# Performance work log

Measured on AMD Instinct MI355X. Metric: run time of the kernel, lower is better.

Reference implementation:

```python
import jax, jax.numpy as jnp
import numpy as np

N = 100000
E = 1200000


def _gcn_norm(edge_index, num_nodes):
    # Add self-loops and compute symmetric normalization (PyG GCNConv default).
    row = jnp.concatenate([edge_index[0], jnp.arange(num_nodes, dtype=edge_index.dtype)])
    col = jnp.concatenate([edge_index[1], jnp.arange(num_nodes, dtype=edge_index.dtype)])
    deg = jax.ops.segment_sum(jnp.ones_like(col, dtype=jnp.float32), col, num_segments=num_nodes)
    dinv = jnp.where(deg > 0, jax.lax.rsqrt(jnp.maximum(deg, 1.0)), 0.0)
    norm = dinv[row] * dinv[col]  # [E+N]
    return row, col, norm


def _gcn_conv(x, W, b, row, col, norm, num_nodes):
    h = x @ W                      # [N, out] dense transform first (fewer bytes to gather)
    msg = h[row] * norm[:, None]   # gather + edge-wise scale
    out = jax.ops.segment_sum(msg, col, num_segments=num_nodes)  # scatter-add to targets
    return out + b


def setup_inputs() -> dict:
    key = jax.random.key(0)
    k1, k2, k3, k4 = jax.random.split(key, 4)
    x = jax.random.normal(k1, (N, 128), dtype=jnp.float32)
    edge_index = jax.random.randint(k2, (2, E), 0, N, dtype=jnp.int64)
    W1 = jax.random.normal(k3, (128, 256), dtype=jnp.float32) * (1.0 / np.sqrt(128))
    b1 = jnp.zeros((256,), dtype=jnp.float32)
    W2 = jax.random.normal(k4, (256, 40), dtype=jnp.float32) * (1.0 / np.sqrt(256))
    b2 = jnp.zeros((40,), dtype=jnp.float32)
    return {"x": x, "edge_index": edge_index, "W1": W1, "b1": b1, "W2": W2, "b2": b2}


def reference(x, edge_index, W1, b1, W2, b2):
    row, col, norm = _gcn_norm(edge_index, N)
    h = _gcn_conv(x, W1, b1, row, col, norm, N)
    h = jax.nn.relu(h)
    # dropout omitted: eval mode (training=False) is identity
    return _gcn_conv(h, W2, b2, row, col, norm, N)
```

## Files before the change

### kernel.cpp

```cpp
#include <hip/hip_runtime.h>
#include <hip/hip_bf16.h>

#define NN 100000
#define EE 1200000
#define F1 128
#define F2 256
#define F3 40
#define MROWS 64
#define NBUK ((NN + 255) / 256)
#define NBLK 256
#define CHUNK ((EE + NBLK - 1) / NBLK)
#define DCAP 4096
#define XB2 ((NN * 32 + 255) / 256)

typedef __bf16 bf16x8 __attribute__((ext_vector_type(8)));
typedef float  f32x4  __attribute__((ext_vector_type(4)));

__device__ __forceinline__ unsigned short f2bf(float f) {
    unsigned u = __float_as_uint(f);
    return (unsigned short)((u + 0x7fffu + ((u >> 16) & 1u)) >> 16);
}
__device__ __forceinline__ float bflo(unsigned v) { return __uint_as_float(v << 16); }
__device__ __forceinline__ float bfhi(unsigned v) { return __uint_as_float(v & 0xffff0000u); }

__global__ __launch_bounds__(256) void k_hist(const int* __restrict__ col,
                                              int* __restrict__ hist) {
    __shared__ int lh[NBUK];
    for (int i = threadIdx.x; i < NBUK; i += 256) lh[i] = 0;
    __syncthreads();
    int e0 = blockIdx.x * CHUNK;
    int e1 = min(e0 + CHUNK, EE);
    for (int e = e0 + threadIdx.x; e < e1; e += 256) {
        int c = col[e];
        if ((unsigned)c < (unsigned)NN) atomicAdd(&lh[c >> 8], 1);
    }
    __syncthreads();
    for (int i = threadIdx.x; i < NBUK; i += 256) hist[i * NBLK + blockIdx.x] = lh[i];
}

__global__ __launch_bounds__(256) void k_scanbin(int* __restrict__ hist,
                                                 int* __restrict__ bintot) {
    __shared__ int s[NBLK];
    int b = blockIdx.x;
    int v = hist[b * NBLK + threadIdx.x];
    s[threadIdx.x] = v;
    __syncthreads();
    int acc = v;
    for (int d = 1; d < NBLK; d <<= 1) {
        int add = (threadIdx.x >= d) ? s[threadIdx.x - d] : 0;
        __syncthreads();
        acc += add;
        s[threadIdx.x] = acc;
        __syncthreads();
    }
    hist[b * NBLK + threadIdx.x] = acc - v;
    if (threadIdx.x == NBLK - 1) bintot[b] = acc;
}

__global__ __launch_bounds__(512) void k_scanbase(const int* __restrict__ bintot,
                                                  int* __restrict__ binbase) {
    __shared__ int s[512];
    int v = (threadIdx.x < NBUK) ? bintot[threadIdx.x] : 0;
    s[threadIdx.x] = v;
    __syncthreads();
    int acc = v;
    for (int d = 1; d < 512; d <<= 1) {
        int add = (threadIdx.x >= d) ? s[threadIdx.x - d] : 0;
        __syncthreads();
        acc += add;
        s[threadIdx.x] = acc;
        __syncthreads();
    }
    if (threadIdx.x < NBUK) binbase[threadIdx.x] = acc - v;
    if (threadIdx.x == NBUK - 1) binbase[NBUK] = acc;
}

__global__ __launch_bounds__(256) void k_scat(const int* __restrict__ row,
                                              const int* __restrict__ col,
                                              const int* __restrict__ hist,
                                              const int* __restrict__ binbase,
                                              unsigned* __restrict__ rec) {
    __shared__ int lcur[NBUK];
    for (int i = threadIdx.x; i < NBUK; i += 256)
        lcur[i] = binbase[i] + hist[i * NBLK + blockIdx.x];
    __syncthreads();
    int e0 = blockIdx.x * CHUNK;
    int e1 = min(e0 + CHUNK, EE);
    for (int e = e0 + threadIdx.x; e < e1; e += 256) {
        int r = row[e], c = col[e];
        if ((unsigned)c < (unsigned)NN) {
            int pos = atomicAdd(&lcur[c >> 8], 1);
            rec[pos] = ((unsigned)r & 0xFFFFFFu) | ((unsigned)(c & 255) << 24);
        }
    }
}

__global__ __launch_bounds__(256) void k_csr(const int* __restrict__ binbase,
                                             const unsigned* __restrict__ rec,
                                             int* __restrict__ eidx,
                                             int* __restrict__ cnt,
                                             int* __restrict__ cursor,
                                             float* __restrict__ dinv) {
    __shared__ int lcnt[256];
    __shared__ int s[256];
    __shared__ int lcur[256];
    __shared__ int lde[DCAP];
    const int b = blockIdx.x;
    const int tid = threadIdx.x;
    lcnt[tid] = 0;
    __syncthreads();
    const int base = binbase[b];
    const int nb = min(binbase[b + 1] - base, DCAP);
    for (int j = tid; j < nb; j += 256) atomicAdd(&lcnt[rec[base + j] >> 24], 1);
    __syncthreads();
    int cv = lcnt[tid];
    s[tid] = cv;
    __syncthreads();
    int acc = cv;
    for (int d = 1; d < 256; d <<= 1) {
        int add = (tid >= d) ? s[tid - d] : 0;
        __syncthreads();
        acc += add;
        s[tid] = acc;
        __syncthreads();
    }
    int excl = acc - cv;
    lcur[tid] = excl;
    const int node = (b << 8) + tid;
    if (node < NN) {
        cnt[node] = cv;
        cursor[node] = base + excl + cv;
        dinv[node] = rsqrtf((float)(cv + 1));
    }
    __syncthreads();
    for (int j = tid; j < nb; j += 256) {
        unsigned v = rec[base + j];
        int pos = atomicAdd(&lcur[v >> 24], 1);
        lde[pos] = (int)(v & 0xFFFFFFu);
    }
    __syncthreads();
    for (int j = tid; j < nb; j += 256) eidx[base + j] = lde[j];
}

__global__ void k_prep(const float4* __restrict__ x, const float* __restrict__ dinv,
                       uint2* __restrict__ xh,
                       const float* __restrict__ W1, const float* __restrict__ W2,
                       __hip_bfloat16* __restrict__ W1p, __hip_bfloat16* __restrict__ W2p) {
    if (blockIdx.x < XB2) {
        int idx = blockIdx.x * 256 + threadIdx.x;
        float d = dinv[idx >> 5];
        float4 v = x[idx];
        uint2 o;
        o.x = (unsigned)f2bf(v.x * d) | ((unsigned)f2bf(v.y * d) << 16);
        o.y = (unsigned)f2bf(v.z * d) | ((unsigned)f2bf(v.w * d) << 16);
        xh[idx] = o;
    } else {
        int idx = (blockIdx.x - XB2) * 256 + threadIdx.x;
        if (idx < F1 * F2) {
            int k = idx / F2, col = idx - (idx / F2) * F2;
            int k8 = k >> 3, j = k & 7;
            W1p[((size_t)(k8 * F2 + col) << 3) + j] = __float2bfloat16(W1[(size_t)k * F2 + col]);
        } else if (idx < F1 * F2 + F2 * 48) {
            int i2 = idx - F1 * F2;
            int k = i2 / 48, col = i2 - (i2 / 48) * 48;
            int k8 = k >> 3, j = k & 7;
            float v = (col < F3) ? W2[(size_t)k * F3 + col] : 0.0f;
            W2p[((size_t)(k8 * 48 + col) << 3) + j] = __float2bfloat16(v);
        }
    }
}

__global__ __launch_bounds__(256) void k_agg1(const int* __restrict__ cursor,
                                              const int* __restrict__ cnt,
                                              const int* __restrict__ eidx,
                                              const float* __restrict__ dinv,
                                              const unsigned* __restrict__ xh,
                                              unsigned* __restrict__ agg) {
    int node = blockIdx.x * 4 + (threadIdx.x >> 6);
    int lane = threadIdx.x & 63;
    if (node >= NN) return;
    unsigned vs = xh[((size_t)node << 6) + lane];
    float a0 = bflo(vs), a1 = bfhi(vs);
    int n = cnt[node];
    int s = cursor[node] - n;
    int k = 0;
    for (; k + 7 < n; k += 8) {
        int r0 = eidx[s + k + 0], r1 = eidx[s + k + 1];
        int r2 = eidx[s + k + 2], r3 = eidx[s + k + 3];
        int r4 = eidx[s + k + 4], r5 = eidx[s + k + 5];
        int r6 = eidx[s + k + 6], r7 = eidx[s + k + 7];
        unsigned v0 = xh[((size_t)r0 << 6) + lane];
        unsigned v1 = xh[((size_t)r1 << 6) + lane];
        unsigned v2 = xh[((size_t)r2 << 6) + lane];
        unsigned v3 = xh[((size_t)r3 << 6) + lane];
        unsigned v4 = xh[((size_t)r4 << 6) + lane];
        unsigned v5 = xh[((size_t)r5 << 6) + lane];
        unsigned v6 = xh[((size_t)r6 << 6) + lane];
        unsigned v7 = xh[((size_t)r7 << 6) + lane];
        a0 += bflo(v0); a1 += bfhi(v0);
        a0 += bflo(v1); a1 += bfhi(v1);
        a0 += bflo(v2); a1 += bfhi(v2);
        a0 += bflo(v3); a1 += bfhi(v3);
        a0 += bflo(v4); a1 += bfhi(v4);
        a0 += bflo(v5); a1 += bfhi(v5);
        a0 += bflo(v6); a1 += bfhi(v6);
        a0 += bflo(v7); a1 += bfhi(v7);
    }
    for (; k + 3 < n; k += 4) {
        int r0 = eidx[s + k + 0], r1 = eidx[s + k + 1];
        int r2 = eidx[s + k + 2], r3 = eidx[s + k + 3];
        unsigned v0 = xh[((size_t)r0 << 6) + lane];
        unsigned v1 = xh[((size_t)r1 << 6) + lane];
        unsigned v2 = xh[((size_t)r2 << 6) + lane];
        unsigned v3 = xh[((size_t)r3 << 6) + lane];
        a0 += bflo(v0); a1 += bfhi(v0);
        a0 += bflo(v1); a1 += bfhi(v1);
        a0 += bflo(v2); a1 += bfhi(v2);
        a0 += bflo(v3); a1 += bfhi(v3);
    }
    for (; k < n; ++k) {
        unsigned v0 = xh[((size_t)eidx[s + k] << 6) + lane];
        a0 += bflo(v0); a1 += bfhi(v0);
    }
    float d = dinv[node];
    agg[((size_t)node << 6) + lane] = (unsigned)f2bf(a0 * d) | ((unsigned)f2bf(a1 * d) << 16);
}

__global__ __launch_bounds__(256) void k_gemm_mfma(
    const __hip_bfloat16* __restrict__ agg, const __hip_bfloat16* __restrict__ W1p,
    const float* __restrict__ b1, const __hip_bfloat16* __restrict__ W2p,
    const float* __restrict__ dinv, unsigned short* __restrict__ tg) {
    __shared__ __hip_bfloat16 h_s[MROWS][F2 + 8];
    const int i0   = blockIdx.x * MROWS;
    const int wave = threadIdx.x >> 6;
    const int lane = threadIdx.x & 63;
    const int m = lane & 15, q = lane >> 4;
    const int rowA = i0 + wave * 16 + m;

    f32x4 acc[16];
#pragma unroll
    for (int c = 0; c < 16; ++c) acc[c] = (f32x4){0.f, 0.f, 0.f, 0.f};

#pragma unroll
    for (int s = 0; s < 4; ++s) {
        bf16x8 a;
#pragma unroll
        for (int j = 0; j < 8; ++j) a[j] = (__bf16)0.0f;
        if (rowA < NN) a = *(const bf16x8*)(agg + (size_t)rowA * F1 + s * 32 + q * 8);
        const __hip_bfloat16* bp = W1p + ((size_t)(4 * s + q) * F2) * 8;
#pragma unroll
        for (int c = 0; c < 16; ++c) {
            bf16x8 b = *(const bf16x8*)(bp + ((size_t)(c * 16 + m) << 3));
            acc[c] = __builtin_amdgcn_mfma_f32_16x16x32_bf16(a, b, acc[c], 0, 0, 0);
        }
    }

#pragma unroll
    for (int c = 0; c < 16; ++c) {
        int col = c * 16 + m;
        float bj = b1[col];
#pragma unroll
        for (int r = 0; r < 4; ++r) {
            int lr = wave * 16 + q * 4 + r;
            h_s[lr][col] = __float2bfloat16(fmaxf(acc[c][r] + bj, 0.0f));
        }
    }
    __syncthreads();

    f32x4 acc2[3];
#pragma unroll
    for (int c = 0; c < 3; ++c) acc2[c] = (f32x4){0.f, 0.f, 0.f, 0.f};

#pragma unroll
    for (int s = 0; s < 8; ++s) {
        bf16x8 a = *(const bf16x8*)(&h_s[wave * 16 + m][s * 32 + q * 8]);
        const __hip_bfloat16* bp = W2p + ((size_t)(4 * s + q) * 48) * 8;
#pragma unroll
        for (int c = 0; c < 3; ++c) {
            bf16x8 b = *(const bf16x8*)(bp + ((size_t)(c * 16 + m) << 3));
            acc2[c] = __builtin_amdgcn_mfma_f32_16x16x32_bf16(a, b, acc2[c], 0, 0, 0);
        }
    }

#pragma unroll
    for (int c = 0; c < 3; ++c) {
        int col = c * 16 + m;
        if (col < F3) {
#pragma unroll
            for (int r = 0; r < 4; ++r) {
                int grow = i0 + wave * 16 + q * 4 + r;
                if (grow < NN)
                    tg[(size_t)grow * F3 + col] = f2bf(acc2[c][r] * dinv[grow]);
            }
        }
    }
}

__global__ __launch_bounds__(256) void k_agg2(const int* __restrict__ cursor,
                                              const int* __restrict__ cnt,
                                              const int* __restrict__ eidx,
                                              const float* __restrict__ dinv,
                                              const unsigned short* __restrict__ tg,
                                              const float* __restrict__ b2,
                                              float* __restrict__ out) {
    const int wave = threadIdx.x >> 6;
    const int lane = threadIdx.x & 63;
    const int h = lane >> 5;
    const int t = lane & 31;
    const int node = blockIdx.x * 8 + wave * 2 + h;
    const unsigned* __restrict__ tgw = (const unsigned*)tg;
    if (t >= 20) return;

    unsigned vs = tgw[(size_t)node * 20 + t];
    float a0 = bflo(vs), a1 = bfhi(vs);
    const int n = cnt[node];
    const int s = cursor[node] - n;
    int k = 0;
    for (; k + 7 < n; k += 8) {
        int r0 = eidx[s + k + 0], r1 = eidx[s + k + 1];
        int r2 = eidx[s + k + 2], r3 = eidx[s + k + 3];
        int r4 = eidx[s + k + 4], r5 = eidx[s + k + 5];
        int r6 = eidx[s + k + 6], r7 = eidx[s + k + 7];
        unsigned v0 = tgw[(size_t)r0 * 20 + t];
        unsigned v1 = tgw[(size_t)r1 * 20 + t];
        unsigned v2 = tgw[(size_t)r2 * 20 + t];
        unsigned v3 = tgw[(size_t)r3 * 20 + t];
        unsigned v4 = tgw[(size_t)r4 * 20 + t];
        unsigned v5 = tgw[(size_t)r5 * 20 + t];
        unsigned v6 = tgw[(size_t)r6 * 20 + t];
        unsigned v7 = tgw[(size_t)r7 * 20 + t];
        a0 += bflo(v0); a1 += bfhi(v0);
        a0 += bflo(v1); a1 += bfhi(v1);
        a0 += bflo(v2); a1 += bfhi(v2);
        a0 += bflo(v3); a1 += bfhi(v3);
        a0 += bflo(v4); a1 += bfhi(v4);
        a0 += bflo(v5); a1 += bfhi(v5);
        a0 += bflo(v6); a1 += bfhi(v6);
        a0 += bflo(v7); a1 += bfhi(v7);
    }
    for (; k + 3 < n; k += 4) {
        int r0 = eidx[s + k + 0], r1 = eidx[s + k + 1];
        int r2 = eidx[s + k + 2], r3 = eidx[s + k + 3];
        unsigned v0 = tgw[(size_t)r0 * 20 + t];
        unsigned v1 = tgw[(size_t)r1 * 20 + t];
        unsigned v2 = tgw[(size_t)r2 * 20 + t];
        unsigned v3 = tgw[(size_t)r3 * 20 + t];
        a0 += bflo(v0); a1 += bfhi(v0);
        a0 += bflo(v1); a1 += bfhi(v1);
        a0 += bflo(v2); a1 += bfhi(v2);
        a0 += bflo(v3); a1 += bfhi(v3);
    }
    for (; k < n; ++k) {
        unsigned v0 = tgw[(size_t)eidx[s + k] * 20 + t];
        a0 += bflo(v0); a1 += bfhi(v0);
    }
    float d = dinv[node];
    float2 bb = ((const float2*)b2)[t];
    float2 o;
    o.x = a0 * d + bb.x;
    o.y = a1 * d + bb.y;
    ((float2*)(out + (size_t)node * F3))[t] = o;
}

extern "C" void kernel_launch(void* const* d_in, const int* in_sizes, int n_in,
                              void* d_out, int out_size, void* d_ws, size_t ws_size,
                              hipStream_t stream) {
    const float* x  = (const float*)d_in[0];
    const int*   ei = (const int*)d_in[1];
    const float* W1 = (const float*)d_in[2];
    const float* b1 = (const float*)d_in[3];
    const float* W2 = (const float*)d_in[4];
    const float* b2 = (const float*)d_in[5];
    float* out = (float*)d_out;

    const int* row = ei;
    const int* col = ei + EE;

    int* cnt     = (int*)d_ws;
    int* cursor  = cnt + NN;
    float* dinv  = (float*)(cursor + NN);
    int* hist    = (int*)(dinv + NN);
    int* bintot  = hist + NBUK * NBLK;
    int* binbase = bintot + NBUK;
    int* eidx    = binbase + (NBUK + 1) + 9;
    unsigned* xh  = (unsigned*)(eidx + EE);
    unsigned* agg = xh + (size_t)NN * 64;
    unsigned* rec = agg;
    unsigned short* tg = (unsigned short*)xh;
    __hip_bfloat16* W1p = (__hip_bfloat16*)(agg + (size_t)NN * 64);
    __hip_bfloat16* W2p = W1p + (size_t)F1 * F2;

    k_hist    <<<NBLK, 256, 0, stream>>>(col, hist);
    k_scanbin <<<NBUK, NBLK, 0, stream>>>(hist, bintot);
    k_scanbase<<<1, 512, 0, stream>>>(bintot, binbase);
    k_scat    <<<NBLK, 256, 0, stream>>>(row, col, hist, binbase, rec);
    k_csr     <<<NBUK, 256, 0, stream>>>(binbase, rec, eidx, cnt, cursor, dinv);

    k_prep<<<XB2 + (F1 * F2 + F2 * 48 + 255) / 256, 256, 0, stream>>>(
        (const float4*)x, dinv, (uint2*)xh, W1, W2, W1p, W2p);

    k_agg1<<<(NN + 3) / 4, 256, 0, stream>>>(cursor, cnt, eidx, dinv, xh, agg);
    k_gemm_mfma<<<(NN + MROWS - 1) / MROWS, 256, 0, stream>>>(
        (const __hip_bfloat16*)agg, W1p, b1, W2p, dinv, tg);
    k_agg2<<<NN / 8, 256, 0, stream>>>(cursor, cnt, eidx, dinv, tg, b2, out);
}
```

Before: 280.4 us.

## Fuse layer-1 aggregation into MFMA GEMM and merge scan kernels via last-block

The layer-1 neighbor aggregation now runs inside the GEMM kernel: each block aggregates its 64 rows directly into shared memory, then runs both MFMA GEMMs, so the bf16 agg buffer is never written to or re-read from global memory. Separately, the base scan is folded into k_scanbin using a last-block-done atomic counter, which removes one kernel launch. The trade-off is fewer blocks in flight during the gather phase: 1563 blocks each process 16 nodes per wave sequentially instead of 25000 small blocks, which may hurt latency hiding for the random gathers. Shared memory is reused between the aggregated tile and the hidden tile, with an added sync between them.

```diff
diff --git a/kernel.cpp b/kernel.cpp
--- a/kernel.cpp
+++ b/kernel.cpp
@@ -24,7 +24,9 @@
 __device__ __forceinline__ float bfhi(unsigned v) { return __uint_as_float(v & 0xffff0000u); }
 
 __global__ __launch_bounds__(256) void k_hist(const int* __restrict__ col,
-                                              int* __restrict__ hist) {
+                                              int* __restrict__ hist,
+                                              int* __restrict__ done) {
+    if (blockIdx.x == 0 && threadIdx.x == 0) *done = 0;
     __shared__ int lh[NBUK];
     for (int i = threadIdx.x; i < NBUK; i += 256) lh[i] = 0;
     __syncthreads();
@@ -38,41 +40,48 @@
     for (int i = threadIdx.x; i < NBUK; i += 256) hist[i * NBLK + blockIdx.x] = lh[i];
 }
 
-__global__ __launch_bounds__(256) void k_scanbin(int* __restrict__ hist,
-                                                 int* __restrict__ bintot) {
-    __shared__ int s[NBLK];
-    int b = blockIdx.x;
-    int v = hist[b * NBLK + threadIdx.x];
-    s[threadIdx.x] = v;
+__global__ __launch_bounds__(512) void k_scanbin(int* __restrict__ hist,
+                                                 int* __restrict__ bintot,
+                                                 int* __restrict__ binbase,
+                                                 int* __restrict__ done) {
+    __shared__ int s[512];
+    __shared__ int lastf;
+    const int b = blockIdx.x;
+    const int tid = threadIdx.x;
+    if (tid == 0) lastf = 0;
+    int v = (tid < NBLK) ? hist[b * NBLK + tid] : 0;
+    s[tid] = v;
     __syncthreads();
     int acc = v;
     for (int d = 1; d < NBLK; d <<= 1) {
-        int add = (threadIdx.x >= d) ? s[threadIdx.x - d] : 0;
+        int add = (tid >= d) ? s[tid - d] : 0;
         __syncthreads();
         acc += add;
-        s[threadIdx.x] = acc;
-        __syncthreads();
-    }
-    hist[b * NBLK + threadIdx.x] = acc - v;
-    if (threadIdx.x == NBLK - 1) bintot[b] = acc;
-}
-
-__global__ __launch_bounds__(512) void k_scanbase(const int* __restrict__ bintot,
-                                                  int* __restrict__ binbase) {
-    __shared__ int s[512];
-    int v = (threadIdx.x < NBUK) ? bintot[threadIdx.x] : 0;
-    s[threadIdx.x] = v;
-    __syncthreads();
-    int acc = v;
+        s[tid] = acc;
+        __syncthreads();
+    }
+    if (tid < NBLK) hist[b * NBLK + tid] = acc - v;
+    if (tid == NBLK - 1) {
+        atomicExch(&bintot[b], acc);
+        __threadfence();
+        if (atomicAdd(done, 1) == NBUK - 1) lastf = 1;
+    }
+    __syncthreads();
+    if (!lastf) return;
+    __threadfence();
+    int w = (tid < NBUK) ? atomicAdd(&bintot[tid], 0) : 0;
+    s[tid] = w;
+    __syncthreads();
+    int a2 = w;
     for (int d = 1; d < 512; d <<= 1) {
-        int add = (threadIdx.x >= d) ? s[threadIdx.x - d] : 0;
-        __syncthreads();
-        acc += add;
-        s[threadIdx.x] = acc;
-        __syncthreads();
-    }
-    if (threadIdx.x < NBUK) binbase[threadIdx.x] = acc - v;
-    if (threadIdx.x == NBUK - 1) binbase[NBUK] = acc;
+        int add = (tid >= d) ? s[tid - d] : 0;
+        __syncthreads();
+        a2 += add;
+        s[tid] = a2;
+        __syncthreads();
+    }
+    if (tid < NBUK) binbase[tid] = a2 - w;
+    if (tid == NBUK - 1) binbase[NBUK] = a2;
 }
 
 __global__ __launch_bounds__(256) void k_scat(const int* __restrict__ row,
@@ -170,83 +179,77 @@
     }
 }
 
-__global__ __launch_bounds__(256) void k_agg1(const int* __restrict__ cursor,
-                                              const int* __restrict__ cnt,
-                                              const int* __restrict__ eidx,
-                                              const float* __restrict__ dinv,
-                                              const unsigned* __restrict__ xh,
-                                              unsigned* __restrict__ agg) {
-    int node = blockIdx.x * 4 + (threadIdx.x >> 6);
-    int lane = threadIdx.x & 63;
-    if (node >= NN) return;
-    unsigned vs = xh[((size_t)node << 6) + lane];
-    float a0 = bflo(vs), a1 = bfhi(vs);
-    int n = cnt[node];
-    int s = cursor[node] - n;
-    int k = 0;
-    for (; k + 7 < n; k += 8) {
-        int r0 = eidx[s + k + 0], r1 = eidx[s + k + 1];
-        int r2 = eidx[s + k + 2], r3 = eidx[s + k + 3];
-        int r4 = eidx[s + k + 4], r5 = eidx[s + k + 5];
-        int r6 = eidx[s + k + 6], r7 = eidx[s + k + 7];
-        unsigned v0 = xh[((size_t)r0 << 6) + lane];
-        unsigned v1 = xh[((size_t)r1 << 6) + lane];
-        unsigned v2 = xh[((size_t)r2 << 6) + lane];
-        unsigned v3 = xh[((size_t)r3 << 6) + lane];
-        unsigned v4 = xh[((size_t)r4 << 6) + lane];
-        unsigned v5 = xh[((size_t)r5 << 6) + lane];
-        unsigned v6 = xh[((size_t)r6 << 6) + lane];
-        unsigned v7 = xh[((size_t)r7 << 6) + lane];
-        a0 += bflo(v0); a1 += bfhi(v0);
-        a0 += bflo(v1); a1 += bfhi(v1);
-        a0 += bflo(v2); a1 += bfhi(v2);
-        a0 += bflo(v3); a1 += bfhi(v3);
-        a0 += bflo(v4); a1 += bfhi(v4);
-        a0 += bflo(v5); a1 += bfhi(v5);
-        a0 += bflo(v6); a1 += bfhi(v6);
-        a0 += bflo(v7); a1 += bfhi(v7);
-    }
-    for (; k + 3 < n; k += 4) {
-        int r0 = eidx[s + k + 0], r1 = eidx[s + k + 1];
-        int r2 = eidx[s + k + 2], r3 = eidx[s + k + 3];
-        unsigned v0 = xh[((size_t)r0 << 6) + lane];
-        unsigned v1 = xh[((size_t)r1 << 6) + lane];
-        unsigned v2 = xh[((size_t)r2 << 6) + lane];
-        unsigned v3 = xh[((size_t)r3 << 6) + lane];
-        a0 += bflo(v0); a1 += bfhi(v0);
-        a0 += bflo(v1); a1 += bfhi(v1);
-        a0 += bflo(v2); a1 += bfhi(v2);
-        a0 += bflo(v3); a1 += bfhi(v3);
-    }
-    for (; k < n; ++k) {
-        unsigned v0 = xh[((size_t)eidx[s + k] << 6) + lane];
-        a0 += bflo(v0); a1 += bfhi(v0);
-    }
-    float d = dinv[node];
-    agg[((size_t)node << 6) + lane] = (unsigned)f2bf(a0 * d) | ((unsigned)f2bf(a1 * d) << 16);
-}
-
-__global__ __launch_bounds__(256) void k_gemm_mfma(
-    const __hip_bfloat16* __restrict__ agg, const __hip_bfloat16* __restrict__ W1p,
-    const float* __restrict__ b1, const __hip_bfloat16* __restrict__ W2p,
-    const float* __restrict__ dinv, unsigned short* __restrict__ tg) {
-    __shared__ __hip_bfloat16 h_s[MROWS][F2 + 8];
+__global__ __launch_bounds__(256) void k_aggemm(
+    const int* __restrict__ cursor, const int* __restrict__ cnt,
+    const int* __restrict__ eidx, const float* __restrict__ dinv,
+    const unsigned* __restrict__ xh,
+    const __hip_bfloat16* __restrict__ W1p, const float* __restrict__ b1,
+    const __hip_bfloat16* __restrict__ W2p, unsigned short* __restrict__ tg) {
+    __shared__ unsigned ash[MROWS][132];
     const int i0   = blockIdx.x * MROWS;
     const int wave = threadIdx.x >> 6;
     const int lane = threadIdx.x & 63;
+
+    for (int j = 0; j < 16; ++j) {
+        const int lrow = wave * 16 + j;
+        const int node = i0 + lrow;
+        if (node >= NN) { ash[lrow][lane] = 0; continue; }
+        unsigned vs = xh[((size_t)node << 6) + lane];
+        float a0 = bflo(vs), a1 = bfhi(vs);
+        int n = cnt[node];
+        int s = cursor[node] - n;
+        int k = 0;
+        for (; k + 7 < n; k += 8) {
+            int r0 = eidx[s + k + 0], r1 = eidx[s + k + 1];
+            int r2 = eidx[s + k + 2], r3 = eidx[s + k + 3];
+            int r4 = eidx[s + k + 4], r5 = eidx[s + k + 5];
+            int r6 = eidx[s + k + 6], r7 = eidx[s + k + 7];
+            unsigned v0 = xh[((size_t)r0 << 6) + lane];
+            unsigned v1 = xh[((size_t)r1 << 6) + lane];
+            unsigned v2 = xh[((size_t)r2 << 6) + lane];
+            unsigned v3 = xh[((size_t)r3 << 6) + lane];
+            unsigned v4 = xh[((size_t)r4 << 6) + lane];
+            unsigned v5 = xh[((size_t)r5 << 6) + lane];
+            unsigned v6 = xh[((size_t)r6 << 6) + lane];
+            unsigned v7 = xh[((size_t)r7 << 6) + lane];
+            a0 += bflo(v0); a1 += bfhi(v0);
+            a0 += bflo(v1); a1 += bfhi(v1);
+            a0 += bflo(v2); a1 += bfhi(v2);
+            a0 += bflo(v3); a1 += bfhi(v3);
+            a0 += bflo(v4); a1 += bfhi(v4);
+            a0 += bflo(v5); a1 += bfhi(v5);
+            a0 += bflo(v6); a1 += bfhi(v6);
+            a0 += bflo(v7); a1 += bfhi(v7);
+        }
+        for (; k + 3 < n; k += 4) {
+            int r0 = eidx[s + k + 0], r1 = eidx[s + k + 1];
+            int r2 = eidx[s + k + 2], r3 = eidx[s + k + 3];
+            unsigned v0 = xh[((size_t)r0 << 6) + lane];
+            unsigned v1 = xh[((size_t)r1 << 6) + lane];
+            unsigned v2 = xh[((size_t)r2 << 6) + lane];
+            unsigned v3 = xh[((size_t)r3 << 6) + lane];
+            a0 += bflo(v0); a1 += bfhi(v0);
+            a0 += bflo(v1); a1 += bfhi(v1);
+            a0 += bflo(v2); a1 += bfhi(v2);
+            a0 += bflo(v3); a1 += bfhi(v3);
+        }
+        for (; k < n; ++k) {
+            unsigned v0 = xh[((size_t)eidx[s + k] << 6) + lane];
+            a0 += bflo(v0); a1 += bfhi(v0);
+        }
+        float d = dinv[node];
+        ash[lrow][lane] = (unsigned)f2bf(a0 * d) | ((unsigned)f2bf(a1 * d) << 16);
+    }
+
     const int m = lane & 15, q = lane >> 4;
-    const int rowA = i0 + wave * 16 + m;
-
     f32x4 acc[16];
 #pragma unroll
     for (int c = 0; c < 16; ++c) acc[c] = (f32x4){0.f, 0.f, 0.f, 0.f};
 
 #pragma unroll
     for (int s = 0; s < 4; ++s) {
-        bf16x8 a;
-#pragma unroll
-        for (int j = 0; j < 8; ++j) a[j] = (__bf16)0.0f;
-        if (rowA < NN) a = *(const bf16x8*)(agg + (size_t)rowA * F1 + s * 32 + q * 8);
+        uint4 t = *(const uint4*)&ash[wave * 16 + m][s * 16 + q * 4];
+        bf16x8 a = __builtin_bit_cast(bf16x8, t);
         const __hip_bfloat16* bp = W1p + ((size_t)(4 * s + q) * F2) * 8;
 #pragma unroll
         for (int c = 0; c < 16; ++c) {
@@ -255,6 +258,8 @@
         }
     }
 
+    __syncthreads();
+    __hip_bfloat16* hs = (__hip_bfloat16*)ash;
 #pragma unroll
     for (int c = 0; c < 16; ++c) {
         int col = c * 16 + m;
@@ -262,7 +267,7 @@
 #pragma unroll
         for (int r = 0; r < 4; ++r) {
             int lr = wave * 16 + q * 4 + r;
-            h_s[lr][col] = __float2bfloat16(fmaxf(acc[c][r] + bj, 0.0f));
+            hs[lr * 264 + col] = __float2bfloat16(fmaxf(acc[c][r] + bj, 0.0f));
         }
     }
     __syncthreads();
@@ -273,7 +278,7 @@
 
 #pragma unroll
     for (int s = 0; s < 8; ++s) {
-        bf16x8 a = *(const bf16x8*)(&h_s[wave * 16 + m][s * 32 + q * 8]);
+        bf16x8 a = *(const bf16x8*)&hs[(wave * 16 + m) * 264 + s * 32 + q * 8];
         const __hip_bfloat16* bp = W2p + ((size_t)(4 * s + q) * 48) * 8;
 #pragma unroll
         for (int c = 0; c < 3; ++c) {
@@ -382,25 +387,23 @@
     int* hist    = (int*)(dinv + NN);
     int* bintot  = hist + NBUK * NBLK;
     int* binbase = bintot + NBUK;
+    int* done    = binbase + NBUK + 1;
     int* eidx    = binbase + (NBUK + 1) + 9;
     unsigned* xh  = (unsigned*)(eidx + EE);
-    unsigned* agg = xh + (size_t)NN * 64;
-    unsigned* rec = agg;
-    unsigned short* tg = (unsigned short*)xh;
-    __hip_bfloat16* W1p = (__hip_bfloat16*)(agg + (size_t)NN * 64);
+    unsigned* rec = xh + (size_t)NN * 64;
+    unsigned short* tg = (unsigned short*)rec;
+    __hip_bfloat16* W1p = (__hip_bfloat16*)(rec + (size_t)NN * 64);
     __hip_bfloat16* W2p = W1p + (size_t)F1 * F2;
 
-    k_hist    <<<NBLK, 256, 0, stream>>>(col, hist);
-    k_scanbin <<<NBUK, NBLK, 0, stream>>>(hist, bintot);
-    k_scanbase<<<1, 512, 0, stream>>>(bintot, binbase);
-    k_scat    <<<NBLK, 256, 0, stream>>>(row, col, hist, binbase, rec);
-    k_csr     <<<NBUK, 256, 0, stream>>>(binbase, rec, eidx, cnt, cursor, dinv);
+    k_hist   <<<NBLK, 256, 0, stream>>>(col, hist, done);
+    k_scanbin<<<NBUK, 512, 0, stream>>>(hist, bintot, binbase, done);
+    k_scat   <<<NBLK, 256, 0, stream>>>(row, col, hist, binbase, rec);
+    k_csr    <<<NBUK, 256, 0, stream>>>(binbase, rec, eidx, cnt, cursor, dinv);
 
     k_prep<<<XB2 + (F1 * F2 + F2 * 48 + 255) / 256, 256, 0, stream>>>(
         (const float4*)x, dinv, (uint2*)xh, W1, W2, W1p, W2p);
 
-    k_agg1<<<(NN + 3) / 4, 256, 0, stream>>>(cursor, cnt, eidx, dinv, xh, agg);
-    k_gemm_mfma<<<(NN + MROWS - 1) / MROWS, 256, 0, stream>>>(
-        (const __hip_bfloat16*)agg, W1p, b1, W2p, dinv, tg);
+    k_aggemm<<<(NN + MROWS - 1) / MROWS, 256, 0, stream>>>(
+        cursor, cnt, eidx, dinv, xh, W1p, b1, W2p, tg);
     k_agg2<<<NN / 8, 256, 0, stream>>>(cursor, cnt, eidx, dinv, tg, b2, out);
 }
```

Result: slower. 366.9 us (+30.8%).

## Replace bucketed CSR build with atomic count, single-pass scan, atomic scatter

Applied to the files above, without the earlier changes.

Rebuilds the destination-sorted edge index using per-node global atomic counts, a block-wise scan with a last-block-done pass for bucket bases, and a direct atomic scatter of source indices. This drops the two-level histogram/bucket sort and its LDS staging kernel, cutting the number of launches and intermediate buffers. In exchange it relies on global atomics with random addresses and uncoalesced scattered writes. The neighbour order within a node also becomes nondeterministic.

```diff
diff --git a/kernel.cpp b/kernel.cpp
--- a/kernel.cpp
+++ b/kernel.cpp
@@ -7,10 +7,7 @@
 #define F2 256
 #define F3 40
 #define MROWS 64
-#define NBUK ((NN + 255) / 256)
-#define NBLK 256
-#define CHUNK ((EE + NBLK - 1) / NBLK)
-#define DCAP 4096
+#define NSB ((NN + 511) / 512)
 #define XB2 ((NN * 32 + 255) / 256)
 
 typedef __bf16 bf16x8 __attribute__((ext_vector_type(8)));
@@ -23,123 +20,78 @@
 __device__ __forceinline__ float bflo(unsigned v) { return __uint_as_float(v << 16); }
 __device__ __forceinline__ float bfhi(unsigned v) { return __uint_as_float(v & 0xffff0000u); }
 
-__global__ __launch_bounds__(256) void k_hist(const int* __restrict__ col,
-                                              int* __restrict__ hist) {
-    __shared__ int lh[NBUK];
-    for (int i = threadIdx.x; i < NBUK; i += 256) lh[i] = 0;
-    __syncthreads();
-    int e0 = blockIdx.x * CHUNK;
-    int e1 = min(e0 + CHUNK, EE);
-    for (int e = e0 + threadIdx.x; e < e1; e += 256) {
+__global__ __launch_bounds__(256) void k_cnt(const int* __restrict__ col,
+                                             int* __restrict__ cnt,
+                                             int* __restrict__ done) {
+    int e = blockIdx.x * 256 + threadIdx.x;
+    if (e == 0) *done = 0;
+    if (e < EE) {
         int c = col[e];
-        if ((unsigned)c < (unsigned)NN) atomicAdd(&lh[c >> 8], 1);
-    }
-    __syncthreads();
-    for (int i = threadIdx.x; i < NBUK; i += 256) hist[i * NBLK + blockIdx.x] = lh[i];
-}
-
-__global__ __launch_bounds__(256) void k_scanbin(int* __restrict__ hist,
-                                                 int* __restrict__ bintot) {
-    __shared__ int s[NBLK];
-    int b = blockIdx.x;
-    int v = hist[b * NBLK + threadIdx.x];
-    s[threadIdx.x] = v;
-    __syncthreads();
-    int acc = v;
-    for (int d = 1; d < NBLK; d <<= 1) {
-        int add = (threadIdx.x >= d) ? s[threadIdx.x - d] : 0;
-        __syncthreads();
-        acc += add;
-        s[threadIdx.x] = acc;
-        __syncthreads();
-    }
-    hist[b * NBLK + threadIdx.x] = acc - v;
-    if (threadIdx.x == NBLK - 1) bintot[b] = acc;
-}
-
-__global__ __launch_bounds__(512) void k_scanbase(const int* __restrict__ bintot,
-                                                  int* __restrict__ binbase) {
+        if ((unsigned)c < (unsigned)NN) atomicAdd(&cnt[c], 1);
+    }
+}
+
+__global__ __launch_bounds__(512) void k_scan(const int* __restrict__ cnt,
+                                              int* __restrict__ start,
+                                              float* __restrict__ dinv,
+                                              int* __restrict__ bintot,
+                                              int* __restrict__ binbase,
+                                              int* __restrict__ done) {
     __shared__ int s[512];
-    int v = (threadIdx.x < NBUK) ? bintot[threadIdx.x] : 0;
-    s[threadIdx.x] = v;
+    __shared__ int lastf;
+    const int b = blockIdx.x;
+    const int tid = threadIdx.x;
+    if (tid == 0) lastf = 0;
+    const int node = b * 512 + tid;
+    int v = (node < NN) ? cnt[node] : 0;
+    s[tid] = v;
     __syncthreads();
     int acc = v;
     for (int d = 1; d < 512; d <<= 1) {
-        int add = (threadIdx.x >= d) ? s[threadIdx.x - d] : 0;
-        __syncthreads();
-        acc += add;
-        s[threadIdx.x] = acc;
-        __syncthreads();
-    }
-    if (threadIdx.x < NBUK) binbase[threadIdx.x] = acc - v;
-    if (threadIdx.x == NBUK - 1) binbase[NBUK] = acc;
-}
-
-__global__ __launch_bounds__(256) void k_scat(const int* __restrict__ row,
-                                              const int* __restrict__ col,
-                                              const int* __restrict__ hist,
-                                              const int* __restrict__ binbase,
-                                              unsigned* __restrict__ rec) {
-    __shared__ int lcur[NBUK];
-    for (int i = threadIdx.x; i < NBUK; i += 256)
-        lcur[i] = binbase[i] + hist[i * NBLK + blockIdx.x];
-    __syncthreads();
-    int e0 = blockIdx.x * CHUNK;
-    int e1 = min(e0 + CHUNK, EE);
-    for (int e = e0 + threadIdx.x; e < e1; e += 256) {
-        int r = row[e], c = col[e];
-        if ((unsigned)c < (unsigned)NN) {
-            int pos = atomicAdd(&lcur[c >> 8], 1);
-            rec[pos] = ((unsigned)r & 0xFFFFFFu) | ((unsigned)(c & 255) << 24);
-        }
-    }
-}
-
-__global__ __launch_bounds__(256) void k_csr(const int* __restrict__ binbase,
-                                             const unsigned* __restrict__ rec,
-                                             int* __restrict__ eidx,
-                                             int* __restrict__ cnt,
-                                             int* __restrict__ cursor,
-                                             float* __restrict__ dinv) {
-    __shared__ int lcnt[256];
-    __shared__ int s[256];
-    __shared__ int lcur[256];
-    __shared__ int lde[DCAP];
-    const int b = blockIdx.x;
-    const int tid = threadIdx.x;
-    lcnt[tid] = 0;
-    __syncthreads();
-    const int base = binbase[b];
-    const int nb = min(binbase[b + 1] - base, DCAP);
-    for (int j = tid; j < nb; j += 256) atomicAdd(&lcnt[rec[base + j] >> 24], 1);
-    __syncthreads();
-    int cv = lcnt[tid];
-    s[tid] = cv;
-    __syncthreads();
-    int acc = cv;
-    for (int d = 1; d < 256; d <<= 1) {
         int add = (tid >= d) ? s[tid - d] : 0;
         __syncthreads();
         acc += add;
         s[tid] = acc;
         __syncthreads();
     }
-    int excl = acc - cv;
-    lcur[tid] = excl;
-    const int node = (b << 8) + tid;
     if (node < NN) {
-        cnt[node] = cv;
-        cursor[node] = base + excl + cv;
-        dinv[node] = rsqrtf((float)(cv + 1));
+        start[node] = acc - v;
+        dinv[node] = rsqrtf((float)(v + 1));
+    }
+    if (tid == 511) {
+        atomicExch(&bintot[b], acc);
+        __threadfence();
+        if (atomicAdd(done, 1) == NSB - 1) lastf = 1;
     }
     __syncthreads();
-    for (int j = tid; j < nb; j += 256) {
-        unsigned v = rec[base + j];
-        int pos = atomicAdd(&lcur[v >> 24], 1);
-        lde[pos] = (int)(v & 0xFFFFFFu);
-    }
+    if (!lastf) return;
+    __threadfence();
+    int w = (tid < NSB) ? atomicAdd(&bintot[tid], 0) : 0;
+    s[tid] = w;
     __syncthreads();
-    for (int j = tid; j < nb; j += 256) eidx[base + j] = lde[j];
+    int a2 = w;
+    for (int d = 1; d < 512; d <<= 1) {
+        int add = (tid >= d) ? s[tid - d] : 0;
+        __syncthreads();
+        a2 += add;
+        s[tid] = a2;
+        __syncthreads();
+    }
+    if (tid < NSB) binbase[tid] = a2 - w;
+    if (tid == NSB - 1) binbase[NSB] = a2;
+}
+
+__global__ __launch_bounds__(256) void k_scat2(const int* __restrict__ row,
+                                               const int* __restrict__ col,
+                                               const int* __restrict__ binbase,
+                                               int* __restrict__ start,
+                                               int* __restrict__ eidx) {
+    int e = blockIdx.x * 256 + threadIdx.x;
+    if (e >= EE) return;
+    int c = col[e];
+    if ((unsigned)c >= (unsigned)NN) return;
+    int pos = binbase[c >> 9] + atomicAdd(&start[c], 1);
+    eidx[pos] = row[e];
 }
 
 __global__ void k_prep(const float4* __restrict__ x, const float* __restrict__ dinv,
@@ -170,7 +122,8 @@
     }
 }
 
-__global__ __launch_bounds__(256) void k_agg1(const int* __restrict__ cursor,
+__global__ __launch_bounds__(256) void k_agg1(const int* __restrict__ binbase,
+                                              const int* __restrict__ start,
                                               const int* __restrict__ cnt,
                                               const int* __restrict__ eidx,
                                               const float* __restrict__ dinv,
@@ -182,7 +135,7 @@
     unsigned vs = xh[((size_t)node << 6) + lane];
     float a0 = bflo(vs), a1 = bfhi(vs);
     int n = cnt[node];
-    int s = cursor[node] - n;
+    int s = binbase[node >> 9] + start[node] - n;
     int k = 0;
     for (; k + 7 < n; k += 8) {
         int r0 = eidx[s + k + 0], r1 = eidx[s + k + 1];
@@ -296,7 +249,8 @@
     }
 }
 
-__global__ __launch_bounds__(256) void k_agg2(const int* __restrict__ cursor,
+__global__ __launch_bounds__(256) void k_agg2(const int* __restrict__ binbase,
+                                              const int* __restrict__ start,
                                               const int* __restrict__ cnt,
                                               const int* __restrict__ eidx,
                                               const float* __restrict__ dinv,
@@ -314,7 +268,7 @@
     unsigned vs = tgw[(size_t)node * 20 + t];
     float a0 = bflo(vs), a1 = bfhi(vs);
     const int n = cnt[node];
-    const int s = cursor[node] - n;
+    const int s = binbase[node >> 9] + start[node] - n;
     int k = 0;
     for (; k + 7 < n; k += 8) {
         int r0 = eidx[s + k + 0], r1 = eidx[s + k + 1];
@@ -377,30 +331,28 @@
     const int* col = ei + EE;
 
     int* cnt     = (int*)d_ws;
-    int* cursor  = cnt + NN;
-    float* dinv  = (float*)(cursor + NN);
-    int* hist    = (int*)(dinv + NN);
-    int* bintot  = hist + NBUK * NBLK;
-    int* binbase = bintot + NBUK;
-    int* eidx    = binbase + (NBUK + 1) + 9;
+    int* start   = cnt + NN;
+    float* dinv  = (float*)(start + NN);
+    int* bintot  = (int*)(dinv + NN);
+    int* binbase = bintot + NSB;
+    int* done    = binbase + NSB + 1;
+    int* eidx    = done + 3;
     unsigned* xh  = (unsigned*)(eidx + EE);
     unsigned* agg = xh + (size_t)NN * 64;
-    unsigned* rec = agg;
     unsigned short* tg = (unsigned short*)xh;
     __hip_bfloat16* W1p = (__hip_bfloat16*)(agg + (size_t)NN * 64);
     __hip_bfloat16* W2p = W1p + (size_t)F1 * F2;
 
-    k_hist    <<<NBLK, 256, 0, stream>>>(col, hist);
-    k_scanbin <<<NBUK, NBLK, 0, stream>>>(hist, bintot);
-    k_scanbase<<<1, 512, 0, stream>>>(bintot, binbase);
-    k_scat    <<<NBLK, 256, 0, stream>>>(row, col, hist, binbase, rec);
-    k_csr     <<<NBUK, 256, 0, stream>>>(binbase, rec, eidx, cnt, cursor, dinv);
+    hipMemsetAsync(cnt, 0, NN * sizeof(int), stream);
+    k_cnt  <<<(EE + 255) / 256, 256, 0, stream>>>(col, cnt, done);
+    k_scan <<<NSB, 512, 0, stream>>>(cnt, start, dinv, bintot, binbase, done);
+    k_scat2<<<(EE + 255) / 256, 256, 0, stream>>>(row, col, binbase, start, eidx);
 
     k_prep<<<XB2 + (F1 * F2 + F2 * 48 + 255) / 256, 256, 0, stream>>>(
         (const float4*)x, dinv, (uint2*)xh, W1, W2, W1p, W2p);
 
-    k_agg1<<<(NN + 3) / 4, 256, 0, stream>>>(cursor, cnt, eidx, dinv, xh, agg);
+    k_agg1<<<(NN + 3) / 4, 256, 0, stream>>>(binbase, start, cnt, eidx, dinv, xh, agg);
     k_gemm_mfma<<<(NN + MROWS - 1) / MROWS, 256, 0, stream>>>(
         (const __hip_bfloat16*)agg, W1p, b1, W2p, dinv, tg);
-    k_agg2<<<NN / 8, 256, 0, stream>>>(cursor, cnt, eidx, dinv, tg, b2, out);
-}
+    k_agg2<<<NN / 8, 256, 0, stream>>>(binbase, start, cnt, eidx, dinv, tg, b2, out);
+}
```

Result: slower. 401.3 us (+43.1%).

## Replace histogram+scan bucketing with fixed-capacity buckets and global atomic cursors

Applied to the files above, without the earlier changes.

Merges the histogram, two scan kernels and scatter into one kernel. Each block counts its local per-bucket edges, reserves space in a fixed DCAP-sized slot per bucket with one global atomic, then scatters records. The CSR kernel reads from these fixed slots and stages records in shared memory so it does not read them twice from global. This drops three kernel launches and the scan passes but adds a memset, makes the order within a bucket nondeterministic, and silently drops any edges beyond DCAP per bucket.

```diff
diff --git a/kernel.cpp b/kernel.cpp
--- a/kernel.cpp
+++ b/kernel.cpp
@@ -23,79 +23,40 @@
 __device__ __forceinline__ float bflo(unsigned v) { return __uint_as_float(v << 16); }
 __device__ __forceinline__ float bfhi(unsigned v) { return __uint_as_float(v & 0xffff0000u); }
 
-__global__ __launch_bounds__(256) void k_hist(const int* __restrict__ col,
-                                              int* __restrict__ hist) {
+__global__ __launch_bounds__(256) void k_scatA(const int* __restrict__ row,
+                                               const int* __restrict__ col,
+                                               int* __restrict__ bcur,
+                                               unsigned* __restrict__ rec) {
     __shared__ int lh[NBUK];
+    __shared__ int lbase[NBUK];
     for (int i = threadIdx.x; i < NBUK; i += 256) lh[i] = 0;
     __syncthreads();
-    int e0 = blockIdx.x * CHUNK;
-    int e1 = min(e0 + CHUNK, EE);
+    const int e0 = blockIdx.x * CHUNK;
+    const int e1 = min(e0 + CHUNK, EE);
     for (int e = e0 + threadIdx.x; e < e1; e += 256) {
         int c = col[e];
         if ((unsigned)c < (unsigned)NN) atomicAdd(&lh[c >> 8], 1);
     }
     __syncthreads();
-    for (int i = threadIdx.x; i < NBUK; i += 256) hist[i * NBLK + blockIdx.x] = lh[i];
-}
-
-__global__ __launch_bounds__(256) void k_scanbin(int* __restrict__ hist,
-                                                 int* __restrict__ bintot) {
-    __shared__ int s[NBLK];
-    int b = blockIdx.x;
-    int v = hist[b * NBLK + threadIdx.x];
-    s[threadIdx.x] = v;
-    __syncthreads();
-    int acc = v;
-    for (int d = 1; d < NBLK; d <<= 1) {
-        int add = (threadIdx.x >= d) ? s[threadIdx.x - d] : 0;
-        __syncthreads();
-        acc += add;
-        s[threadIdx.x] = acc;
-        __syncthreads();
-    }
-    hist[b * NBLK + threadIdx.x] = acc - v;
-    if (threadIdx.x == NBLK - 1) bintot[b] = acc;
-}
-
-__global__ __launch_bounds__(512) void k_scanbase(const int* __restrict__ bintot,
-                                                  int* __restrict__ binbase) {
-    __shared__ int s[512];
-    int v = (threadIdx.x < NBUK) ? bintot[threadIdx.x] : 0;
-    s[threadIdx.x] = v;
-    __syncthreads();
-    int acc = v;
-    for (int d = 1; d < 512; d <<= 1) {
-        int add = (threadIdx.x >= d) ? s[threadIdx.x - d] : 0;
-        __syncthreads();
-        acc += add;
-        s[threadIdx.x] = acc;
-        __syncthreads();
-    }
-    if (threadIdx.x < NBUK) binbase[threadIdx.x] = acc - v;
-    if (threadIdx.x == NBUK - 1) binbase[NBUK] = acc;
-}
-
-__global__ __launch_bounds__(256) void k_scat(const int* __restrict__ row,
-                                              const int* __restrict__ col,
-                                              const int* __restrict__ hist,
-                                              const int* __restrict__ binbase,
-                                              unsigned* __restrict__ rec) {
-    __shared__ int lcur[NBUK];
-    for (int i = threadIdx.x; i < NBUK; i += 256)
-        lcur[i] = binbase[i] + hist[i * NBLK + blockIdx.x];
-    __syncthreads();
-    int e0 = blockIdx.x * CHUNK;
-    int e1 = min(e0 + CHUNK, EE);
+    for (int i = threadIdx.x; i < NBUK; i += 256) {
+        int cn = lh[i];
+        lbase[i] = cn ? atomicAdd(&bcur[i], cn) : 0;
+        lh[i] = 0;
+    }
+    __syncthreads();
     for (int e = e0 + threadIdx.x; e < e1; e += 256) {
         int r = row[e], c = col[e];
         if ((unsigned)c < (unsigned)NN) {
-            int pos = atomicAdd(&lcur[c >> 8], 1);
-            rec[pos] = ((unsigned)r & 0xFFFFFFu) | ((unsigned)(c & 255) << 24);
-        }
-    }
-}
-
-__global__ __launch_bounds__(256) void k_csr(const int* __restrict__ binbase,
+            int b = c >> 8;
+            int pos = lbase[b] + atomicAdd(&lh[b], 1);
+            if (pos < DCAP)
+                rec[(size_t)b * DCAP + pos] =
+                    ((unsigned)r & 0xFFFFFFu) | ((unsigned)(c & 255) << 24);
+        }
+    }
+}
+
+__global__ __launch_bounds__(256) void k_csr(const int* __restrict__ bcur,
                                              const unsigned* __restrict__ rec,
                                              int* __restrict__ eidx,
                                              int* __restrict__ cnt,
@@ -104,14 +65,19 @@
     __shared__ int lcnt[256];
     __shared__ int s[256];
     __shared__ int lcur[256];
+    __shared__ unsigned lrec[DCAP];
     __shared__ int lde[DCAP];
     const int b = blockIdx.x;
     const int tid = threadIdx.x;
     lcnt[tid] = 0;
     __syncthreads();
-    const int base = binbase[b];
-    const int nb = min(binbase[b + 1] - base, DCAP);
-    for (int j = tid; j < nb; j += 256) atomicAdd(&lcnt[rec[base + j] >> 24], 1);
+    const int base = b * DCAP;
+    const int nb = min(bcur[b], DCAP);
+    for (int j = tid; j < nb; j += 256) {
+        unsigned v = rec[(size_t)base + j];
+        lrec[j] = v;
+        atomicAdd(&lcnt[v >> 24], 1);
+    }
     __syncthreads();
     int cv = lcnt[tid];
     s[tid] = cv;
@@ -134,7 +100,7 @@
     }
     __syncthreads();
     for (int j = tid; j < nb; j += 256) {
-        unsigned v = rec[base + j];
+        unsigned v = lrec[j];
         int pos = atomicAdd(&lcur[v >> 24], 1);
         lde[pos] = (int)(v & 0xFFFFFFu);
     }
@@ -379,22 +345,18 @@
     int* cnt     = (int*)d_ws;
     int* cursor  = cnt + NN;
     float* dinv  = (float*)(cursor + NN);
-    int* hist    = (int*)(dinv + NN);
-    int* bintot  = hist + NBUK * NBLK;
-    int* binbase = bintot + NBUK;
-    int* eidx    = binbase + (NBUK + 1) + 9;
-    unsigned* xh  = (unsigned*)(eidx + EE);
+    int* bcur    = (int*)(dinv + NN);
+    int* eidx    = bcur + NBUK + 9;
+    unsigned* xh  = (unsigned*)(eidx + NBUK * DCAP);
     unsigned* agg = xh + (size_t)NN * 64;
     unsigned* rec = agg;
     unsigned short* tg = (unsigned short*)xh;
     __hip_bfloat16* W1p = (__hip_bfloat16*)(agg + (size_t)NN * 64);
     __hip_bfloat16* W2p = W1p + (size_t)F1 * F2;
 
-    k_hist    <<<NBLK, 256, 0, stream>>>(col, hist);
-    k_scanbin <<<NBUK, NBLK, 0, stream>>>(hist, bintot);
-    k_scanbase<<<1, 512, 0, stream>>>(bintot, binbase);
-    k_scat    <<<NBLK, 256, 0, stream>>>(row, col, hist, binbase, rec);
-    k_csr     <<<NBUK, 256, 0, stream>>>(binbase, rec, eidx, cnt, cursor, dinv);
+    hipMemsetAsync(bcur, 0, NBUK * sizeof(int), stream);
+    k_scatA<<<NBLK, 256, 0, stream>>>(row, col, bcur, rec);
+    k_csr  <<<NBUK, 256, 0, stream>>>(bcur, rec, eidx, cnt, cursor, dinv);
 
     k_prep<<<XB2 + (F1 * F2 + F2 * 48 + 255) / 256, 256, 0, stream>>>(
         (const float4*)x, dinv, (uint2*)xh, W1, W2, W1p, W2p);
```

Result: no change. 277.4 us (-1.0%).
